# Kernel optimization log

Measured on AMD Instinct MI355X. Metric: run time of the kernel, lower is better.

The kernel has to match this reference:

```python
import jax, jax.numpy as jnp
import numpy as np

N_USERS = 27094
M_SPOTS = 42852
D = 128
E_US = 600000
E_SP = 500000
L = 3  # num_layers


def setup_inputs() -> dict:
    key = jax.random.key(0)
    ks = jax.random.split(key, 16)
    spot_emb = jax.random.normal(ks[0], (M_SPOTS, D), jnp.float32) * 0.1
    user_emb = jax.random.normal(ks[1], (N_USERS, D), jnp.float32) * 0.1
    W_spot = jax.random.normal(ks[2], (D, D), jnp.float32) / np.sqrt(D)
    W_spot10 = jax.random.normal(ks[3], (D, D), jnp.float32) / np.sqrt(D)
    W_spot20 = jax.random.normal(ks[4], (D, D), jnp.float32) / np.sqrt(D)
    user_spot = jnp.stack([
        jax.random.randint(ks[5], (E_US,), 0, N_USERS, jnp.int32),
        jax.random.randint(ks[6], (E_US,), 0, M_SPOTS, jnp.int32),
    ])
    def mk_graph(k1, k2, k3):
        ei = jnp.stack([
            jax.random.randint(k1, (E_SP,), 0, M_SPOTS, jnp.int32),
            jax.random.randint(k2, (E_SP,), 0, M_SPOTS, jnp.int32),
        ])
        ew = jax.random.uniform(k3, (E_SP,), jnp.float32)
        return ei, ew
    spot_edge_index, spot_edge_weight = mk_graph(ks[7], ks[8], ks[9])
    spot10_edge_index, spot10_edge_weight = mk_graph(ks[10], ks[11], ks[12])
    spot20_edge_index, spot20_edge_weight = mk_graph(ks[13], ks[14], ks[15])
    return {
        'spot_emb': spot_emb, 'user_emb': user_emb,
        'W_spot': W_spot, 'W_spot10': W_spot10, 'W_spot20': W_spot20,
        'spot_edge_weight': spot_edge_weight, 'spot10_edge_weight': spot10_edge_weight,
        'spot20_edge_weight': spot20_edge_weight,
        'user_spot': user_spot, 'spot_edge_index': spot_edge_index,
        'spot10_edge_index': spot10_edge_index, 'spot20_edge_index': spot20_edge_index,
    }


def _gcn_light(x, W, ei, ew, n):
    # GCNConv semantics with given edge weights, no self loops, no bias:
    # x' = xW; deg = scatter(ew, dst); out = sum_e dinv[src]*ew*dinv[dst] * x'[src]
    xw = x @ W
    deg = jax.ops.segment_sum(ew, ei[1], num_segments=n)
    dinv = jnp.where(deg > 0, jax.lax.rsqrt(jnp.maximum(deg, 1e-12)), 0.0)
    norm = dinv[ei[0]] * ew * dinv[ei[1]]
    return jax.ops.segment_sum(norm[:, None] * xw[ei[0]], ei[1], num_segments=n)


def _propagate(spot_x, user_x, u, s, inv_div):
    # LightGCN bipartite propagation with symmetric sqrt(deg_u*deg_s) norm,
    # accumulating the mean over layer outputs (incl. layer 0).
    spot_acc, user_acc = spot_x, user_x
    for _ in range(L):
        user_new = jax.ops.segment_sum(spot_x[s] * inv_div, u, num_segments=N_USERS)
        spot_new = jax.ops.segment_sum(user_x[u] * inv_div, s, num_segments=M_SPOTS)
        spot_x, user_x = spot_new, user_new
        spot_acc = spot_acc + spot_x
        user_acc = user_acc + user_x
    inv = 1.0 / (L + 1)
    return spot_acc * inv, user_acc * inv, spot_x, user_x


def reference(spot_emb, user_emb, W_spot, W_spot10, W_spot20,
              spot_edge_weight, spot10_edge_weight, spot20_edge_weight,
              user_spot, spot_edge_index, spot10_edge_index, spot20_edge_index):
    u, s = user_spot[0], user_spot[1]
    ones = jnp.ones((u.shape[0],), jnp.float32)
    udeg = jax.ops.segment_sum(ones, u, num_segments=N_USERS)
    sdeg = jax.ops.segment_sum(ones, s, num_segments=M_SPOTS)
    inv_div = (1.0 / jnp.sqrt(udeg[u] * sdeg[s]))[:, None]  # [E_US,1]

    # branch 1: spot_x1 includes the category conv before propagation
    cat1 = _gcn_light(spot_emb, W_spot, spot_edge_index, spot_edge_weight, M_SPOTS)
    so1, uo1, _, _ = _propagate(spot_emb + cat1, user_emb, u, s, inv_div)

    # branches 2 and 3 propagate raw embeddings (conv output only added to the
    # accumulator's layer-0 term in the original code), so share one propagation
    p_s, p_u, fin_s, _ = _propagate(spot_emb, user_emb, u, s, inv_div)
    cat2 = _gcn_light(spot_emb, W_spot10, spot10_edge_index, spot10_edge_weight, M_SPOTS)
    so2 = p_s + cat2 / (L + 1)
    uo2 = p_u
    # original code (faithfully) feeds the post-loop spot_x2 into spot_conv20
    cat3 = _gcn_light(fin_s, W_spot20, spot20_edge_index, spot20_edge_weight, M_SPOTS)
    so3 = p_s + cat3 / (L + 1)
    uo3 = p_u
    return (so1, uo1, so2, uo2, so3, uo3)
```

## Files before the change

### kernel.cpp

```cpp
#include <hip/hip_runtime.h>
#include <hip/hip_fp16.h>

#define D 128
#define RU 64
#define RS 48
#define RG 40
#define CU_CAP 62
#define CS_CAP 46
#define CG_CAP 38
typedef unsigned int uint;
typedef unsigned short ushort;
typedef unsigned long long ull;

__device__ __forceinline__ float blo(uint u) { return __uint_as_float(u << 16); }
__device__ __forceinline__ float bhi(uint u) { return __uint_as_float(u & 0xffff0000u); }
__device__ __forceinline__ uint bpack(float a, float b) {
  uint ua = __float_as_uint(a), ub = __float_as_uint(b);
  ua = (ua + 0x7fffu + ((ua >> 16) & 1u)) >> 16;
  ub = (ub + 0x7fffu + ((ub >> 16) & 1u)) & 0xffff0000u;
  return ua | ub;
}
__device__ __forceinline__ float h2f(ushort h) { return __half2float(__ushort_as_half(h)); }
__device__ __forceinline__ ushort f2h(float f) { return __half_as_ushort(__float2half(f)); }

#define PKSCALE 16777216.0f
#define PKMASK ((1ULL << 40) - 1)

__device__ __forceinline__ float gdinv_of(ull pk) {
  float d = (float)(pk & PKMASK) * (1.0f / PKSCALE);
  return d > 0.f ? rsqrtf(fmaxf(d, 1e-12f)) : 0.f;
}
__device__ __forceinline__ float cdinv(int c) {
  return c > 0 ? rsqrtf((float)c) : 0.f;
}
__device__ __forceinline__ int headcnt(const ushort* rowb) {
  return (int)*(const uint*)rowb;
}

struct SingleTbl { const uint2* p; };
__device__ __forceinline__ float4 ldx(const float* X, size_t i) {
  return ((const float4*)X)[i];
}
__device__ __forceinline__ float4 ldx(SingleTbl X, size_t i) {
  uint2 v = X.p[i];
  return make_float4(blo(v.x), bhi(v.x), blo(v.y), bhi(v.y));
}

template <typename XT>
__device__ __forceinline__ void gemm_body(int blk, XT X, const float* __restrict__ W,
                                          ushort* __restrict__ Y, int rows,
                                          const uint* __restrict__ gheads) {
  int tid = threadIdx.x;
  int c = tid & 31, rg = tid >> 5;
  int r0 = blk * 32 + rg * 4;
  float4 acc[4];
#pragma unroll
  for (int j = 0; j < 4; ++j) acc[j] = make_float4(0.f, 0.f, 0.f, 0.f);
  for (int k4 = 0; k4 < 32; ++k4) {
    float4 xv[4];
#pragma unroll
    for (int j = 0; j < 4; ++j) {
      int r = r0 + j;
      if (r >= rows) r = rows - 1;
      xv[j] = ldx(X, (size_t)r * 32 + k4);
    }
#pragma unroll
    for (int kk = 0; kk < 4; ++kk) {
      float4 wv = ((const float4*)W)[(k4 * 4 + kk) * 32 + c];
#pragma unroll
      for (int j = 0; j < 4; ++j) {
        float xs = kk == 0 ? xv[j].x : kk == 1 ? xv[j].y : kk == 2 ? xv[j].z : xv[j].w;
        acc[j].x = fmaf(xs, wv.x, acc[j].x);
        acc[j].y = fmaf(xs, wv.y, acc[j].y);
        acc[j].z = fmaf(xs, wv.z, acc[j].z);
        acc[j].w = fmaf(xs, wv.w, acc[j].w);
      }
    }
  }
#pragma unroll
  for (int j = 0; j < 4; ++j) {
    int r = r0 + j;
    if (r < rows) {
      float sc = gheads ? gdinv_of(*(const ull*)(gheads + (size_t)r * RG)) : 1.0f;
      ((uint2*)(Y + (size_t)r * D))[c] =
          make_uint2(bpack(sc * acc[j].x, sc * acc[j].y),
                     bpack(sc * acc[j].z, sc * acc[j].w));
    }
  }
}

__global__ __launch_bounds__(256) void k_build(
    const int* __restrict__ uu, const int* __restrict__ ss, int EUS,
    const int* __restrict__ ei1, const int* __restrict__ ei2, const int* __restrict__ ei3,
    const float* __restrict__ ew1, const float* __restrict__ ew2,
    const float* __restrict__ ew3, int ES1, int ES2, int ES3,
    ushort* __restrict__ ue_s, ushort* __restrict__ se_u, uint* __restrict__ grec,
    int M, int nbBip, int nbG,
    const float* __restrict__ se, const float* __restrict__ W1, ushort* __restrict__ xw) {
  int b = blockIdx.x;
  if (b < nbBip) {
    int e = b * 256 + threadIdx.x;
    if (e >= EUS) return;
    int ui = uu[e], si = ss[e];
    uint p = atomicAdd((uint*)(ue_s + (size_t)ui * RU), 1u);
    if (p < CU_CAP) ue_s[(size_t)ui * RU + 2 + p] = (ushort)si;
    uint q = atomicAdd((uint*)(se_u + (size_t)si * RS), 1u);
    if (q < CS_CAP) se_u[(size_t)si * RS + 2 + q] = (ushort)ui;
  } else if (b < nbBip + nbG) {
    int t = (b - nbBip) * 256 + threadIdx.x;
    const int* ei; const float* ew; int g, le, ESg;
    if (t < ES1) { g = 0; le = t; ei = ei1; ew = ew1; ESg = ES1; }
    else if (t < ES1 + ES2) { g = 1; le = t - ES1; ei = ei2; ew = ew2; ESg = ES2; }
    else if (t < ES1 + ES2 + ES3) { g = 2; le = t - ES1 - ES2; ei = ei3; ew = ew3; ESg = ES3; }
    else return;
    int src = ei[le], dst = ei[ESg + le];
    float w = ew[le];
    uint* grow = grec + ((size_t)g * M + dst) * RG;
    ull pk = (1ULL << 40) | (ull)(uint)(w * PKSCALE);
    ull old = atomicAdd((ull*)grow, pk);
    int p = (int)(old >> 40);
    if (p < CG_CAP) grow[2 + p] = (uint)src | ((uint)f2h(w) << 16);
  } else {
    gemm_body(b - nbBip - nbG, se, W1, xw, M, (const uint*)nullptr);
  }
}

__device__ __forceinline__ void gcn_body(int gblk, const uint* __restrict__ gr,
                                         const ushort* __restrict__ xw,
                                         const float* __restrict__ base,
                                         float* __restrict__ out, uint* outSC,
                                         const ushort* __restrict__ se_adj,
                                         float scale, int M, bool neighborDinv) {
  int g = gblk * 256 + threadIdx.x;
  int row = g >> 6, l = g & 63;
  if (row >= M) return;
  const uint* grow = gr + (size_t)row * RG;
  ull mypk = *(const ull*)grow;
  int cv = (int)(mypk >> 40);
  if (cv > CG_CAP) cv = CG_CAP;
  float dr = gdinv_of(mypk);
  const uint* sv = (const uint*)xw;
  float2 sum = make_float2(0.f, 0.f);
#pragma unroll 4
  for (int i = 0; i < cv; ++i) {
    uint rec = grow[2 + i];
    int sr = (int)(rec & 0xffffu);
    float w = h2f((ushort)(rec >> 16));
    if (neighborDinv) w *= gdinv_of(*(const ull*)(gr + (size_t)sr * RG));
    uint v = sv[(size_t)sr * 64 + l];
    sum.x = fmaf(w, blo(v), sum.x);
    sum.y = fmaf(w, bhi(v), sum.y);
  }
  float sc = dr * scale;
  size_t lf = (size_t)row * 64 + l;
  float2 b = ((const float2*)base)[lf];
  float2 o = make_float2(fmaf(sc, sum.x, b.x), fmaf(sc, sum.y, b.y));
  ((float2*)out)[lf] = o;
  if (outSC) {
    float sd = cdinv(headcnt(se_adj + (size_t)row * RS));
    outSC[(size_t)row * 128 + 4 * (l >> 1) + (l & 1)] = bpack(sd * o.x, sd * o.y);
  }
}

__global__ __launch_bounds__(256) void k_mid(
    const uint* __restrict__ grec1, const ushort* __restrict__ xw,
    const float* __restrict__ spot_emb, float* __restrict__ o_so1,
    uint* __restrict__ SC, const ushort* __restrict__ se_u, int M, int nbGg1,
    const float* __restrict__ ue, const ushort* __restrict__ ue_adj,
    uint2* __restrict__ UCs, int N) {
  int b = blockIdx.x;
  if (b < nbGg1) {
    gcn_body(b, grec1, xw, spot_emb, o_so1, SC, se_u, 1.0f, M, true);
    return;
  }
  int g = (b - nbGg1) * 256 + threadIdx.x;
  int row = g >> 5, lane = g & 31;
  if (row < N) {
    float d = cdinv(headcnt(ue_adj + (size_t)row * RU));
    float4 v = ((const float4*)ue)[(size_t)row * 32 + lane];
    UCs[(size_t)row * 32 + lane] =
        make_uint2(bpack(d * v.x, d * v.y), bpack(d * v.z, d * v.w));
  } else if (row < N + M) {
    int r = row - N;
    float d = cdinv(headcnt(se_u + (size_t)r * RS));
    float4 v = ((const float4*)spot_emb)[(size_t)r * 32 + lane];
    ((uint2*)SC)[(size_t)r * 64 + 2 * lane + 1] =
        make_uint2(bpack(d * v.x, d * v.y), bpack(d * v.z, d * v.w));
  }
}

__global__ __launch_bounds__(256) void k_prop(
    const ushort* __restrict__ ue_s, const ushort* __restrict__ se_u,
    const uint2* __restrict__ uG, int uGs,
    const uint2* __restrict__ sG, int sGs,
    uint2* uO, int uOs, uint2* sO, int sOs,
    int finalLayer,
    const uint2* __restrict__ uT1, int uT1s, const uint2* __restrict__ uT2, int uT2s,
    const uint2* __restrict__ sT1, int sT1s, const uint2* __restrict__ sT2, int sT2s,
    const float* __restrict__ bu1, const float* __restrict__ bu2,
    const float* __restrict__ bs1, const float* __restrict__ bs2,
    float* au1, float* au2, float* as1, float* as2, float* du2, float* ds2,
    int N, int M, int nbProp,
    const float* __restrict__ Xg, const float* __restrict__ Wg,
    ushort* __restrict__ xwg, const uint* __restrict__ gheads) {
  int b = blockIdx.x;
  if (b >= nbProp) {
    if (Wg) gemm_body(b - nbProp, Xg, Wg, xwg, M, gheads);
    return;
  }
  int g = b * 256 + threadIdx.x;
  int row = g >> 6, l = g & 63;
  if (row >= N + M) return;
  bool isU = row < N;
  int r = isU ? row : row - N;
  const ushort* rowb = isU ? (ue_s + (size_t)r * RU) : (se_u + (size_t)r * RS);
  int cvf = headcnt(rowb);
  int cap = isU ? CU_CAP : CS_CAP;
  int cv = cvf > cap ? cap : cvf;
  const ushort* ei = rowb + 2;
  const uint2* G = isU ? uG : sG;
  int Gs = isU ? uGs : sGs;
  int j = l >> 1, sig = l & 1;
  float w = cdinv(cvf);
  float4 s = make_float4(0.f, 0.f, 0.f, 0.f);
  if (Gs) {
#pragma unroll 4
    for (int i = 0; i < cv; ++i) {
      uint2 v = G[(size_t)ei[i] * 32 + j];
      s.x += blo(v.x); s.y += bhi(v.x); s.z += blo(v.y); s.w += bhi(v.y);
    }
  } else {
#pragma unroll 4
    for (int i = 0; i < cv; ++i) {
      uint2 v = G[(size_t)ei[i] * 64 + l];
      s.x += blo(v.x); s.y += bhi(v.x); s.z += blo(v.y); s.w += bhi(v.y);
    }
  }
  uint2 v1 = make_uint2(0, 0), v2 = make_uint2(0, 0);
  if (finalLayer) {
    const uint2* T1 = isU ? uT1 : sT1;
    int t1s = isU ? uT1s : sT1s;
    const uint2* T2 = isU ? uT2 : sT2;
    int t2s = isU ? uT2s : sT2s;
    v1 = T1[t1s ? ((size_t)r * 32 + j) : ((size_t)r * 64 + l)];
    v2 = T2[t2s ? ((size_t)r * 32 + j) : ((size_t)r * 64 + l)];
  }
  uint2* O = isU ? uO : sO;
  int Os = isU ? uOs : sOs;
  float f = finalLayer ? w : w * w;
  if (O) {
    uint2 e = make_uint2(bpack(f * s.x, f * s.y), bpack(f * s.z, f * s.w));
    if (Os) {
      if (!sig) O[(size_t)r * 32 + j] = e;
    } else {
      O[(size_t)r * 64 + l] = e;
    }
  }
  if (!finalLayer) return;
  float winv = cvf > 0 ? sqrtf((float)cvf) : 0.f;
  const float* bp = isU ? (sig ? bu2 : bu1) : (sig ? bs2 : bs1);
  float4 base = ((const float4*)bp)[(size_t)r * 32 + j];
  float4 acc;
  acc.x = (base.x + winv * (blo(v1.x) + blo(v2.x)) + w * s.x) * 0.25f;
  acc.y = (base.y + winv * (bhi(v1.x) + bhi(v2.x)) + w * s.y) * 0.25f;
  acc.z = (base.z + winv * (blo(v1.y) + blo(v2.y)) + w * s.z) * 0.25f;
  acc.w = (base.w + winv * (bhi(v1.y) + bhi(v2.y)) + w * s.w) * 0.25f;
  float* ap = isU ? (sig ? au2 : au1) : (sig ? as2 : as1);
  ((float4*)ap)[(size_t)r * 32 + j] = acc;
  float* dp = isU ? du2 : ds2;
  if (sig && dp) ((float4*)dp)[(size_t)r * 32 + j] = acc;
}

__global__ __launch_bounds__(256) void k_tail(
    int gG, SingleTbl X3, const float* __restrict__ W3, ushort* __restrict__ xw3,
    int rows, const uint* __restrict__ grec3, const uint* __restrict__ grec2,
    const ushort* __restrict__ xw2, float* __restrict__ o_so2, float scale, int M) {
  int b = blockIdx.x;
  if (b < gG) gemm_body(b, X3, W3, xw3, rows, grec3);
  else gcn_body(b - gG, grec2, xw2, o_so2, o_so2, (uint*)nullptr,
                (const ushort*)nullptr, scale, M, false);
}

__global__ __launch_bounds__(256) void k_gg(
    const uint* __restrict__ grecg, const ushort* __restrict__ xw,
    const float* __restrict__ base, float* __restrict__ out, float scale, int M) {
  gcn_body(blockIdx.x, grecg, xw, base, out, (uint*)nullptr,
           (const ushort*)nullptr, scale, M, false);
}

extern "C" void kernel_launch(void* const* d_in, const int* in_sizes, int n_in,
                              void* d_out, int out_size, void* d_ws, size_t ws_size,
                              hipStream_t stream) {
  const float* spot_emb = (const float*)d_in[0];
  const float* user_emb = (const float*)d_in[1];
  const float* W1 = (const float*)d_in[2];
  const float* W2 = (const float*)d_in[3];
  const float* W3 = (const float*)d_in[4];
  const float* ew1 = (const float*)d_in[5];
  const float* ew2 = (const float*)d_in[6];
  const float* ew3 = (const float*)d_in[7];
  const int* us = (const int*)d_in[8];
  const int* ei1 = (const int*)d_in[9];
  const int* ei2 = (const int*)d_in[10];
  const int* ei3 = (const int*)d_in[11];

  const int M = in_sizes[0] / D;
  const int N = in_sizes[1] / D;
  const int EUS = in_sizes[8] / 2;
  const int ES1 = in_sizes[9] / 2;
  const int ES2 = in_sizes[10] / 2;
  const int ES3 = in_sizes[11] / 2;
  const int EStot = ES1 + ES2 + ES3;

  const int* uu = us;
  const int* ss = us + EUS;

  const size_t MD = (size_t)M * D, ND = (size_t)N * D;

  float* cur = (float*)d_ws;
  auto take = [&](size_t nfloats) {
    float* p = cur; cur += (nfloats + 63) & ~(size_t)63; return p;
  };

  ushort* ue_s = (ushort*)take((size_t)N * RU / 2);
  ushort* se_u = (ushort*)take((size_t)M * RS / 2);
  uint* grec = (uint*)take((size_t)3 * M * RG);
  float* zero_end = cur;
  ushort* xw = (ushort*)take(MD / 2);
  uint2* UC_A = (uint2*)take(ND);
  uint2* UC_B = (uint2*)take(ND);
  uint2* SC_A = (uint2*)take(MD);
  uint2* SC_B = (uint2*)take(MD);

  ushort* xw3 = (ushort*)UC_A;
  uint2* FIN = SC_B + (size_t)M * 32;
  const uint* grec2 = grec + (size_t)M * RG;
  const uint* grec3 = grec + (size_t)2 * M * RG;

  float* out = (float*)d_out;
  float* o_so1 = out;
  float* o_uo1 = o_so1 + MD;
  float* o_so2 = o_uo1 + ND;
  float* o_uo2 = o_so2 + MD;
  float* o_so3 = o_uo2 + ND;
  float* o_uo3 = o_so3 + MD;

  const int B = 256;
  auto gr = [&](size_t work) { return (int)((work + B - 1) / B); };
  const int nbBip = gr(EUS);
  const int nbG = gr(EStot);
  const int nbPack = gr((size_t)(N + M) * 32);
  const int gProp = gr((size_t)(N + M) * 64);
  const int gM64 = gr((size_t)M * 64);
  const int gG = (M + 31) / 32;
  float* nulf = (float*)nullptr;
  const uint2* nult = (const uint2*)nullptr;

  hipMemsetAsync(ue_s, 0, (char*)zero_end - (char*)ue_s, stream);

  k_build<<<nbBip + nbG + gG, B, 0, stream>>>(
      uu, ss, EUS, ei1, ei2, ei3, ew1, ew2, ew3, ES1, ES2, ES3,
      ue_s, se_u, grec, M, nbBip, nbG, spot_emb, W1, xw);

  k_mid<<<gM64 + nbPack, B, 0, stream>>>(grec, xw, spot_emb, o_so1, (uint*)SC_A,
                                         se_u, M, gM64, user_emb, ue_s, UC_A, N);

  k_prop<<<gProp + gG, B, 0, stream>>>(
      ue_s, se_u, SC_A, 0, UC_A, 1, UC_B, 0, SC_B, 1, 0,
      nult, 0, nult, 0, nult, 0, nult, 0,
      nulf, nulf, nulf, nulf, nulf, nulf, nulf, nulf, nulf, nulf,
      N, M, gProp, spot_emb, W2, xw, grec2);
  k_prop<<<gProp, B, 0, stream>>>(
      ue_s, se_u, SC_B, 1, UC_B, 0, UC_A, 1, SC_A, 0, 0,
      nult, 0, nult, 0, nult, 0, nult, 0,
      nulf, nulf, nulf, nulf, nulf, nulf, nulf, nulf, nulf, nulf,
      N, M, gProp, nulf, nulf, (ushort*)nullptr, (const uint*)nullptr);
  k_prop<<<gProp, B, 0, stream>>>(
      ue_s, se_u, SC_A, 0, UC_A, 1, (uint2*)nullptr, 0, FIN, 1, 1,
      UC_B, 0, UC_A, 1, SC_B, 1, SC_A, 0,
      user_emb, user_emb, o_so1, spot_emb,
      o_uo1, o_uo2, o_so1, o_so2, o_uo3, o_so3,
      N, M, gProp, nulf, nulf, (ushort*)nullptr, (const uint*)nullptr);

  k_tail<<<gG + gM64, B, 0, stream>>>(gG, SingleTbl{FIN}, W3, xw3, M,
                                      grec3, grec2, xw, o_so2, 0.25f, M);
  k_gg<<<gM64, B, 0, stream>>>(grec3, xw3, o_so3, o_so3, 0.25f, M);
}
```

Measured before the change: 663.6 us.

## Partition adjacency build by destination residue to localize atomics, widen row caps

The edge-bucketing phase of the build kernel now has each block scan a chunk of 2048 edges and handle only those whose destination index modulo 8 matches its partition. Eight blocks re-read every chunk, and each of them touches only one eighth of the rows, with the aim of improving cache locality and spreading atomic contention. The spot adjacency and graph row capacities are also enlarged (RS 48->64, RG 40->48), which changes the memory footprint and stride. The cost is reading the edge arrays eight times over, plus more branch divergence inside each block.

After: 811.2 us. 1.22x slower.

```diff
diff --git a/kernel.cpp b/kernel.cpp
--- a/kernel.cpp
+++ b/kernel.cpp
@@ -3,11 +3,12 @@
 
 #define D 128
 #define RU 64
-#define RS 48
-#define RG 40
+#define RS 64
+#define RG 48
 #define CU_CAP 62
-#define CS_CAP 46
-#define CG_CAP 38
+#define CS_CAP 62
+#define CG_CAP 46
+#define BCHUNK 2048
 typedef unsigned int uint;
 typedef unsigned short ushort;
 typedef unsigned long long ull;
@@ -99,27 +100,44 @@
     const float* __restrict__ se, const float* __restrict__ W1, ushort* __restrict__ xw) {
   int b = blockIdx.x;
   if (b < nbBip) {
-    int e = b * 256 + threadIdx.x;
-    if (e >= EUS) return;
-    int ui = uu[e], si = ss[e];
-    uint p = atomicAdd((uint*)(ue_s + (size_t)ui * RU), 1u);
-    if (p < CU_CAP) ue_s[(size_t)ui * RU + 2 + p] = (ushort)si;
-    uint q = atomicAdd((uint*)(se_u + (size_t)si * RS), 1u);
-    if (q < CS_CAP) se_u[(size_t)si * RS + 2 + q] = (ushort)ui;
+    int part = b & 7;
+    int base = (b >> 3) * BCHUNK;
+#pragma unroll
+    for (int k = 0; k < BCHUNK / 256; ++k) {
+      int e = base + k * 256 + threadIdx.x;
+      if (e >= EUS) continue;
+      int ui = uu[e], si = ss[e];
+      if ((ui & 7) == part) {
+        uint p = atomicAdd((uint*)(ue_s + (size_t)ui * RU), 1u);
+        if (p < CU_CAP) ue_s[(size_t)ui * RU + 2 + p] = (ushort)si;
+      }
+      if ((si & 7) == part) {
+        uint q = atomicAdd((uint*)(se_u + (size_t)si * RS), 1u);
+        if (q < CS_CAP) se_u[(size_t)si * RS + 2 + q] = (ushort)ui;
+      }
+    }
   } else if (b < nbBip + nbG) {
-    int t = (b - nbBip) * 256 + threadIdx.x;
-    const int* ei; const float* ew; int g, le, ESg;
-    if (t < ES1) { g = 0; le = t; ei = ei1; ew = ew1; ESg = ES1; }
-    else if (t < ES1 + ES2) { g = 1; le = t - ES1; ei = ei2; ew = ew2; ESg = ES2; }
-    else if (t < ES1 + ES2 + ES3) { g = 2; le = t - ES1 - ES2; ei = ei3; ew = ew3; ESg = ES3; }
-    else return;
-    int src = ei[le], dst = ei[ESg + le];
-    float w = ew[le];
-    uint* grow = grec + ((size_t)g * M + dst) * RG;
-    ull pk = (1ULL << 40) | (ull)(uint)(w * PKSCALE);
-    ull old = atomicAdd((ull*)grow, pk);
-    int p = (int)(old >> 40);
-    if (p < CG_CAP) grow[2 + p] = (uint)src | ((uint)f2h(w) << 16);
+    int bb = b - nbBip;
+    int part = bb & 7;
+    int base = (bb >> 3) * BCHUNK;
+#pragma unroll
+    for (int k = 0; k < BCHUNK / 256; ++k) {
+      int t = base + k * 256 + threadIdx.x;
+      const int* ei; const float* ew; int g, le, ESg;
+      if (t < ES1) { g = 0; le = t; ei = ei1; ew = ew1; ESg = ES1; }
+      else if (t < ES1 + ES2) { g = 1; le = t - ES1; ei = ei2; ew = ew2; ESg = ES2; }
+      else if (t < ES1 + ES2 + ES3) { g = 2; le = t - ES1 - ES2; ei = ei3; ew = ew3; ESg = ES3; }
+      else continue;
+      int dst = ei[ESg + le];
+      if ((dst & 7) != part) continue;
+      int src = ei[le];
+      float w = ew[le];
+      uint* grow = grec + ((size_t)g * M + dst) * RG;
+      ull pk = (1ULL << 40) | (ull)(uint)(w * PKSCALE);
+      ull old = atomicAdd((ull*)grow, pk);
+      int p = (int)(old >> 40);
+      if (p < CG_CAP) grow[2 + p] = (uint)src | ((uint)f2h(w) << 16);
+    }
   } else {
     gemm_body(b - nbBip - nbG, se, W1, xw, M, (const uint*)nullptr);
   }
@@ -347,8 +365,8 @@
 
   const int B = 256;
   auto gr = [&](size_t work) { return (int)((work + B - 1) / B); };
-  const int nbBip = gr(EUS);
-  const int nbG = gr(EStot);
+  const int nbBip = (int)(((size_t)EUS + BCHUNK - 1) / BCHUNK) * 8;
+  const int nbG = (int)(((size_t)EStot + BCHUNK - 1) / BCHUNK) * 8;
   const int nbPack = gr((size_t)(N + M) * 32);
   const int gProp = gr((size_t)(N + M) * 64);
   const int gM64 = gr((size_t)M * 64);
```
